# Performance work log

Hardware: AMD Instinct MI355X
Metric: run time of the kernel (lower is better)

## Reference

```python
import jax, jax.numpy as jnp
import numpy as np

EPS = 1.0  # global `epsilon` in the original code
B, C, N, T = 4, 32, 256, 288
NUM_PRED, NUM_LOCAL = 12, 12
PERIOD, SHORT, LONG = 24, 12, 48
EMB = 16
RE_K = 5  # ResidualExtrapolate kernel width (num_input)


def const_extrap(x, p):
    # replicate-pad right by p along time
    return jnp.concatenate([x, jnp.repeat(x[..., -1:], p, axis=-1)], axis=-1)


def seasonal_extrap(x, p):
    # circular-pad right by p along time (p <= t)
    return jnp.concatenate([x, x[..., :p]], axis=-1)


def term_norm(x, L):
    # sliding-window mean/var over last axis, window L, replicate-padded left.
    pad1 = [(0, 0)] * 3 + [(1, 0)]
    cs = jnp.pad(jnp.cumsum(x, axis=-1), pad1)
    cs2 = jnp.pad(jnp.cumsum(x * x, axis=-1), pad1)
    mean = (cs[..., L:] - cs[..., :-L]) / L            # (b,c,n,t-L+1)
    var = (cs2[..., L:] - cs2[..., :-L]) / L - mean ** 2 + 1e-5
    padL = [(0, 0)] * 3 + [(L - 1, 0)]
    mean = jnp.pad(mean, padL, mode='edge')
    var = jnp.pad(var, padL, mode='edge')
    out = (x - mean) / jnp.sqrt(var + EPS)
    return out, mean, jnp.sqrt(var)


def seasonal_norm(x, P):
    b, c, n, t = x.shape
    xp = x.reshape(b, c, n, t // P, P)
    mean = xp.mean(3)                                   # (b,c,n,P) per-phase
    var = (xp ** 2).mean(3) - mean ** 2 + 1e-5
    mean = jnp.tile(mean, (1, 1, 1, t // P))
    var = jnp.tile(var, (1, 1, 1, t // P))
    out = (x - mean) / jnp.sqrt(var + EPS)
    return out, mean, jnp.sqrt(var)


def spatial_norm(x, emb):
    n = emb.shape[0]
    adj = emb @ emb.T - 10.0 * jnp.eye(n, dtype=x.dtype)
    adj = jax.nn.softmax(adj, axis=-1)                  # (n,n)
    mean = jnp.einsum('nm,bcmt->bcnt', adj, x)
    var = jnp.einsum('nm,bcmt->bcnt', adj, x * x) - mean ** 2 + 1e-5
    out = (x - mean) / jnp.sqrt(var + EPS)
    return out, mean, jnp.sqrt(var)


def residual_extrap(x, W, bias):
    # Conv2d(c -> c*num_pred, kernel (1, RE_K)) on last RE_K steps, then cat.
    b, c, n, t = x.shape
    y = jnp.einsum('ock,bcnk->bon', W[:, :, 0, :], x[..., -RE_K:]) + bias[None, :, None]
    proj = y.reshape(b, NUM_PRED, c, n).transpose(0, 2, 3, 1)  # (b,c,n,num_pred)
    return jnp.concatenate([x, proj], axis=-1)


def conv_time(x, W, bias):
    y = jax.lax.conv_general_dilated(x, W, (1, 1), 'VALID',
                                     dimension_numbers=('NCHW', 'OIHW', 'NCHW'))
    return y + bias[None, :, None, None]


def conv1x1(x, W, bias):
    return jnp.einsum('oc,bcnt->bont', W[:, :, 0, 0], x) + bias[None, :, None, None]


def setup_inputs() -> dict:
    key = jax.random.key(0)
    ks = jax.random.split(key, 16)
    f32 = jnp.float32

    def w(k, shape, fan_in):
        return jax.random.normal(k, shape, dtype=f32) / np.sqrt(fan_in)

    inp = {
        'x': jax.random.normal(ks[0], (B, C, N, T), dtype=f32),
        'node_embedding': 0.1 * jax.random.normal(ks[1], (N, EMB), dtype=f32),
        'conv1_w': w(ks[6], (C, 13 * C, 1, NUM_LOCAL), 13 * C * NUM_LOCAL),
        'conv1_b': jnp.zeros((C,), f32),
        'conv2_w': w(ks[7], (C, 13 * C, 1, NUM_LOCAL), 13 * C * NUM_LOCAL),
        'conv2_b': jnp.zeros((C,), f32),
        'skip_w': w(ks[8], (C, C, 1, 1), C),
        'skip_b': jnp.zeros((C,), f32),
        'res_w': w(ks[9], (C, C, 1, 1), C),
        'res_b': jnp.zeros((C,), f32),
    }
    for i in range(4):
        inp[f're{i + 1}_w'] = w(ks[2 + i], (C * NUM_PRED, C, 1, RE_K), C * RE_K)
        inp[f're{i + 1}_b'] = jnp.zeros((C * NUM_PRED,), f32)
    return inp


def reference(x, node_embedding, conv1_w, conv1_b, conv2_w, conv2_b,
              skip_w, skip_b, res_w, res_b,
              re1_w, re1_b, re2_w, re2_b, re3_w, re3_b, re4_w, re4_b):
    xs, aux = [], []

    x_proj = const_extrap(x, NUM_PRED)
    zeros = jnp.zeros_like(x_proj)
    xs.append(x_proj); aux.append(zeros)

    x1, lt_mean, lt_std = term_norm(x, LONG)
    xp = residual_extrap(x1, re1_w, re1_b)
    mp, sp = const_extrap(lt_mean, NUM_PRED), const_extrap(lt_std, NUM_PRED)
    xs += [xp, mp, sp]; aux += [zeros, mp, sp]

    x2, se_mean, se_std = seasonal_norm(x1, PERIOD)
    xp = residual_extrap(x2, re2_w, re2_b)
    mp, sp = seasonal_extrap(se_mean, NUM_PRED), seasonal_extrap(se_std, NUM_PRED)
    xs += [xp, mp, sp]; aux += [zeros, mp, sp]

    x3, st_mean, st_std = term_norm(x2, SHORT)
    xp = residual_extrap(x3, re3_w, re3_b)
    mp, sp = const_extrap(st_mean, NUM_PRED), const_extrap(st_std, NUM_PRED)
    xs += [xp, mp, sp]; aux += [zeros, mp, sp]

    x4, sn_mean, sn_std = spatial_norm(x3, node_embedding)
    xp = residual_extrap(x4, re4_w, re4_b)
    mp, sp = const_extrap(sn_mean, NUM_PRED), const_extrap(sn_std, NUM_PRED)
    xs += [xp, mp, sp]; aux += [zeros, mp, sp]

    pad1 = [(0, 0)] * 3 + [(1, 0)]
    x_cat = jnp.pad(jnp.concatenate(xs, axis=1), pad1)      # (b,13c,n,T+P+1)
    a_cat = jnp.pad(jnp.concatenate(aux, axis=1), pad1)

    g1 = conv_time(x_cat, conv1_w, conv1_b)
    g2 = conv_time(x_cat, conv2_w, conv2_b)
    a1 = conv_time(a_cat, conv1_w, conv1_b)
    a2 = conv_time(a_cat, conv2_w, conv2_b)

    prod = g1 * g2
    x_z = conv1x1(prod[..., :-NUM_PRED], res_w, res_b)
    s = conv1x1(prod[..., -NUM_PRED:], skip_w, skip_b)
    s_aux = conv1x1((a1 * a2)[..., -NUM_PRED:], skip_w, skip_b)
    return (x_z, s_aux, s)
```

## Files before the change

### kernel.cpp

```cpp
#include <hip/hip_runtime.h>

typedef unsigned short u16;
typedef __attribute__((ext_vector_type(8))) short short8v;
typedef __attribute__((ext_vector_type(4))) float f32x4;

#define PSTR 304L
#define OFF_SAUX 9109504L
#define OFF_S    9502720L
#define CHSTR (32L*256L*PSTR)

static __device__ __forceinline__ float bf2f(u16 u) {
  return __uint_as_float(((unsigned int)u) << 16);
}
static __device__ __forceinline__ u16 f2bf(float f) {
  unsigned int i = __float_as_uint(f);
  i += 0x7FFFu + ((i >> 16) & 1u);
  return (u16)(i >> 16);
}

static __device__ __forceinline__ void gload16(const void* g, void* l) {
  __builtin_amdgcn_global_load_lds(
      (const __attribute__((address_space(1))) unsigned int*)g,
      (__attribute__((address_space(3))) unsigned int*)l, 16, 0, 0);
}

static __device__ void adj_body(int row, const float* __restrict__ emb,
                                u16* __restrict__ adjb) {
  const int m = threadIdx.x;
  __shared__ float sred[8];
  float er[16];
#pragma unroll
  for (int e = 0; e < 16; ++e) er[e] = emb[row * 16 + e];
  float d = 0.f;
#pragma unroll
  for (int e = 0; e < 16; ++e) d += er[e] * emb[m * 16 + e];
  if (m == row) d -= 10.f;
  float v = d;
#pragma unroll
  for (int off = 32; off; off >>= 1) v = fmaxf(v, __shfl_xor(v, off, 64));
  const int wid = m >> 6, lane = m & 63;
  if (lane == 0) sred[wid] = v;
  __syncthreads();
  const float mx = fmaxf(fmaxf(sred[0], sred[1]), fmaxf(sred[2], sred[3]));
  const float p = expf(d - mx);
  v = p;
#pragma unroll
  for (int off = 32; off; off >>= 1) v += __shfl_xor(v, off, 64);
  if (lane == 0) sred[4 + wid] = v;
  __syncthreads();
  const float sum = sred[4] + sred[5] + sred[6] + sred[7];
  adjb[row * 256 + m] = f2bf(p / sum);
}

static __device__ void prepw_body(int bid, const float* __restrict__ c1w,
                                  const float* __restrict__ c2w,
                                  u16* __restrict__ wB) {
  const int idx = bid * 256 + threadIdx.x;
  const int kk = idx >> 11;
  const int rem = idx & 2047;
  const int j = rem >> 5, chp = rem & 31;
  const int pslot = chp >> 3, chlo = chp & 7;
  const int sl = pslot ^ ((j >> 1) & 3);
  const int ch = sl * 8 + chlo;
  const int g = kk / 12, k = kk - g * 12;
  const int cin = g * 32 + ch;
  const float* src = (j < 32) ? c1w : c2w;
  const int jj = j & 31;
  wB[idx] = f2bf(src[(jj * 416 + cin) * 12 + k]);
}

static __device__ __forceinline__ void wscan2(float& s1, float& s2, int lane) {
#pragma unroll
  for (int off = 1; off < 64; off <<= 1) {
    float a = __shfl_up(s1, off, 64);
    float b = __shfl_up(s2, off, 64);
    if (lane >= off) { s1 += a; s2 += b; }
  }
}

static __device__ void norm_body(int bid, const float* __restrict__ x,
                                 u16* __restrict__ xcat) {
  const int wid = threadIdx.x >> 6, lane = threadIdx.x & 63;
  const long row = (long)bid * 4 + wid;
  const int b = (int)(row >> 13);
  const int c = (int)((row >> 8) & 31);
  const int n = (int)(row & 255);
  const float* xr = x + row * 288;
  __shared__ float bufA[4][304], bufB[4][304], cs1[4][312], cs2[4][312], sst[4][80];
  float* bA = bufA[wid];
  float* bB = bufB[wid];
  float* p1 = cs1[wid];
  float* p2 = cs2[wid];
  float* psm = sst[wid];
  float* psi = sst[wid] + 24;
  float* psd = sst[wid] + 48;
  const long chb = (long)b * 416 * 256 + n;

  for (int j = 0; j < 5; ++j) { int t = j * 64 + lane; if (t < 288) bA[t] = xr[t]; }

  auto scanbuf = [&](float* src) {
    float ca = 0.f, cb = 0.f;
    if (lane == 0) { p1[0] = 0.f; p2[0] = 0.f; }
    for (int j = 0; j < 5; ++j) {
      int t = j * 64 + lane;
      float v = (t < 288) ? src[t] : 0.f;
      float s1 = v, s2 = v * v;
      wscan2(s1, s2, lane);
      if (t < 288) { p1[t + 1] = ca + s1; p2[t + 1] = cb + s2; }
      ca += __shfl(s1, 63, 64);
      cb += __shfl(s2, 63, 64);
    }
  };

  scanbuf(bA);
  for (int j = 0; j < 5; ++j) {
    int t = j * 64 + lane; if (t >= 288) continue;
    float S, Q;
    if (t >= 47) { S = p1[t + 1] - p1[t - 47]; Q = p2[t + 1] - p2[t - 47]; }
    else         { S = p1[48];                 Q = p2[48]; }
    float m = S * (1.f / 48.f);
    float var = Q * (1.f / 48.f) - m * m + 1e-5f;
    float sd = sqrtf(var);
    float iv = rsqrtf(var + 1.f);
    float xv = bA[t];
    float x1 = (xv - m) * iv;
    bB[t] = x1;
    xcat[(chb + (long)(c)      * 256) * PSTR + 1 + t] = f2bf(xv);
    xcat[(chb + (long)(32 + c) * 256) * PSTR + 1 + t] = f2bf(x1);
    xcat[(chb + (long)(64 + c) * 256) * PSTR + 1 + t] = f2bf(m);
    xcat[(chb + (long)(96 + c) * 256) * PSTR + 1 + t] = f2bf(sd);
  }
  {
    float S = p1[288] - p1[240], Q = p2[288] - p2[240];
    float m = S * (1.f / 48.f);
    float var = Q * (1.f / 48.f) - m * m + 1e-5f;
    float sd = sqrtf(var);
    if (lane < 12) {
      xcat[(chb + (long)(c)      * 256) * PSTR + 289 + lane] = f2bf(bA[287]);
      xcat[(chb + (long)(64 + c) * 256) * PSTR + 289 + lane] = f2bf(m);
      xcat[(chb + (long)(96 + c) * 256) * PSTR + 289 + lane] = f2bf(sd);
    }
    if (lane == 0) {
      xcat[(chb + (long)(c)      * 256) * PSTR] = 0;
      xcat[(chb + (long)(32 + c) * 256) * PSTR] = 0;
      xcat[(chb + (long)(64 + c) * 256) * PSTR] = 0;
      xcat[(chb + (long)(96 + c) * 256) * PSTR] = 0;
    }
  }
  if (lane < 24) {
    float S = 0.f, Q = 0.f;
#pragma unroll
    for (int i2 = 0; i2 < 12; ++i2) { float v = bB[lane + 24 * i2]; S += v; Q += v * v; }
    float m = S * (1.f / 12.f);
    float var = Q * (1.f / 12.f) - m * m + 1e-5f;
    psm[lane] = m; psi[lane] = rsqrtf(var + 1.f); psd[lane] = sqrtf(var);
  }
  for (int j = 0; j < 5; ++j) {
    int t = j * 64 + lane; if (t >= 288) continue;
    int ph = t % 24;
    float m = psm[ph];
    float x2v = (bB[t] - m) * psi[ph];
    bA[t] = x2v;
    xcat[(chb + (long)(128 + c) * 256) * PSTR + 1 + t] = f2bf(x2v);
    xcat[(chb + (long)(160 + c) * 256) * PSTR + 1 + t] = f2bf(m);
    xcat[(chb + (long)(192 + c) * 256) * PSTR + 1 + t] = f2bf(psd[ph]);
  }
  if (lane < 12) {
    xcat[(chb + (long)(160 + c) * 256) * PSTR + 289 + lane] = f2bf(psm[lane]);
    xcat[(chb + (long)(192 + c) * 256) * PSTR + 289 + lane] = f2bf(psd[lane]);
  }
  if (lane == 0) {
    xcat[(chb + (long)(128 + c) * 256) * PSTR] = 0;
    xcat[(chb + (long)(160 + c) * 256) * PSTR] = 0;
    xcat[(chb + (long)(192 + c) * 256) * PSTR] = 0;
  }
  scanbuf(bA);
  for (int j = 0; j < 5; ++j) {
    int t = j * 64 + lane; if (t >= 288) continue;
    float S, Q;
    if (t >= 11) { S = p1[t + 1] - p1[t - 11]; Q = p2[t + 1] - p2[t - 11]; }
    else         { S = p1[12];                 Q = p2[12]; }
    float m = S * (1.f / 12.f);
    float var = Q * (1.f / 12.f) - m * m + 1e-5f;
    float sd = sqrtf(var);
    float iv = rsqrtf(var + 1.f);
    float x3v = (bA[t] - m) * iv;
    xcat[(chb + (long)(224 + c) * 256) * PSTR + 1 + t] = f2bf(x3v);
    xcat[(chb + (long)(256 + c) * 256) * PSTR + 1 + t] = f2bf(m);
    xcat[(chb + (long)(288 + c) * 256) * PSTR + 1 + t] = f2bf(sd);
  }
  {
    float S = p1[288] - p1[276], Q = p2[288] - p2[276];
    float m = S * (1.f / 12.f);
    float var = Q * (1.f / 12.f) - m * m + 1e-5f;
    float sd = sqrtf(var);
    if (lane < 12) {
      xcat[(chb + (long)(256 + c) * 256) * PSTR + 289 + lane] = f2bf(m);
      xcat[(chb + (long)(288 + c) * 256) * PSTR + 289 + lane] = f2bf(sd);
    }
    if (lane == 0) {
      xcat[(chb + (long)(224 + c) * 256) * PSTR] = 0;
      xcat[(chb + (long)(256 + c) * 256) * PSTR] = 0;
      xcat[(chb + (long)(288 + c) * 256) * PSTR] = 0;
    }
  }
}

__global__ __launch_bounds__(256) void k_front(const float* __restrict__ x,
    const float* __restrict__ emb, const float* __restrict__ c1w,
    const float* __restrict__ c2w, u16* __restrict__ xcat,
    u16* __restrict__ adjb, u16* __restrict__ wB) {
  const int bid = blockIdx.x;
  if (bid < 8192)       norm_body(bid, x, xcat);
  else if (bid < 8448)  adj_body(bid - 8192, emb, adjb);
  else                  prepw_body(bid - 8448, c1w, c2w, wB);
}

static __device__ void re_body(long gid, u16* __restrict__ xcat,
                               const float* __restrict__ W,
                               const float* __restrict__ bias, int srcch) {
  const int o = (int)(gid % 384);
  const long bn = gid / 384;
  const int n = (int)(bn & 255);
  const int b = (int)(bn >> 8);
  const float* wr = W + o * 160;
  float acc = bias[o];
  for (int c = 0; c < 32; ++c) {
    const long rb = ((long)(b * 416 + srcch + c) * 256 + n) * PSTR + 284;
#pragma unroll
    for (int k = 0; k < 5; ++k) acc += wr[c * 5 + k] * bf2f(xcat[rb + k]);
  }
  const int cd = o & 31, p = o >> 5;
  xcat[((long)(b * 416 + srcch + cd) * 256 + n) * PSTR + 289 + p] = f2bf(acc);
}

__global__ __launch_bounds__(256) void k_re4(u16* __restrict__ xcat,
                                             const float* __restrict__ W,
                                             const float* __restrict__ bias) {
  re_body((long)blockIdx.x * 256 + threadIdx.x, xcat, W, bias, 320);
}

static __device__ void spatial_body(int sid, u16* __restrict__ xcat,
                                    const u16* __restrict__ adjb) {
  const int gx = sid % 20;
  const int slice = sid / 20;
  const int tcn = gx >> 2, ncb = gx & 3;
  const int b = slice >> 5, c = slice & 31;
  const int t0 = tcn * 64, n0 = ncb * 64;
  const int tid = threadIdx.x;
  const int wid = tid >> 6, lane = tid & 63;
  const int wm = wid >> 1, wn = wid & 1;
  const int l15 = lane & 15, lq = lane >> 4;
  __shared__ __align__(16) u16 BT[2][64 * 40];
  __shared__ __align__(16) u16 BT2[2][64 * 40];
  const f32x4 vz = {0.f, 0.f, 0.f, 0.f};
  f32x4 aM[2][2], aV[2][2];
#pragma unroll
  for (int i = 0; i < 2; ++i)
#pragma unroll
    for (int j = 0; j < 2; ++j) { aM[i][j] = vz; aV[i][j] = vz; }
  const long base7 = (long)(b * 416 + 224 + c) * 256;
  u16 rv[8];
#pragma unroll
  for (int r = 0; r < 8; ++r) {
    int idx = tid + r * 256; int ml = idx >> 6, s = idx & 63;
    rv[r] = xcat[(base7 + ml) * PSTR + 1 + t0 + s];
  }
#pragma unroll
  for (int r = 0; r < 8; ++r) {
    int idx = tid + r * 256; int ml = idx >> 6, s = idx & 63;
    float v = bf2f(rv[r]);
    BT[0][s * 40 + ml] = rv[r];
    BT2[0][s * 40 + ml] = f2bf(v * v);
  }
  __syncthreads();
  int cur = 0;
  for (int kk = 0; kk < 8; ++kk) {
    u16 rn[8];
    if (kk < 7) {
#pragma unroll
      for (int r = 0; r < 8; ++r) {
        int idx = tid + r * 256; int ml = idx >> 6, s = idx & 63;
        rn[r] = xcat[(base7 + (long)((kk + 1) * 32 + ml)) * PSTR + 1 + t0 + s];
      }
    }
    const short8v a0 = *(const short8v*)(adjb + (long)(n0 + wm * 32 + l15) * 256 + kk * 32 + lq * 8);
    const short8v a1 = *(const short8v*)(adjb + (long)(n0 + wm * 32 + 16 + l15) * 256 + kk * 32 + lq * 8);
    const u16* bt = BT[cur];
    const u16* bq = BT2[cur];
    const short8v b0 = *(const short8v*)(bt + (wn * 32 + l15) * 40 + lq * 8);
    const short8v b1 = *(const short8v*)(bt + (wn * 32 + 16 + l15) * 40 + lq * 8);
    const short8v q0 = *(const short8v*)(bq + (wn * 32 + l15) * 40 + lq * 8);
    const short8v q1 = *(const short8v*)(bq + (wn * 32 + 16 + l15) * 40 + lq * 8);
    aM[0][0] = __builtin_amdgcn_mfma_f32_16x16x32_bf16(a0, b0, aM[0][0], 0, 0, 0);
    aM[0][1] = __builtin_amdgcn_mfma_f32_16x16x32_bf16(a0, b1, aM[0][1], 0, 0, 0);
    aM[1][0] = __builtin_amdgcn_mfma_f32_16x16x32_bf16(a1, b0, aM[1][0], 0, 0, 0);
    aM[1][1] = __builtin_amdgcn_mfma_f32_16x16x32_bf16(a1, b1, aM[1][1], 0, 0, 0);
    aV[0][0] = __builtin_amdgcn_mfma_f32_16x16x32_bf16(a0, q0, aV[0][0], 0, 0, 0);
    aV[0][1] = __builtin_amdgcn_mfma_f32_16x16x32_bf16(a0, q1, aV[0][1], 0, 0, 0);
    aV[1][0] = __builtin_amdgcn_mfma_f32_16x16x32_bf16(a1, q0, aV[1][0], 0, 0, 0);
    aV[1][1] = __builtin_amdgcn_mfma_f32_16x16x32_bf16(a1, q1, aV[1][1], 0, 0, 0);
    __syncthreads();
    if (kk < 7) {
#pragma unroll
      for (int r = 0; r < 8; ++r) {
        int idx = tid + r * 256; int ml = idx >> 6, s = idx & 63;
        float v = bf2f(rn[r]);
        BT[cur ^ 1][s * 40 + ml] = rn[r];
        BT2[cur ^ 1][s * 40 + ml] = f2bf(v * v);
      }
    }
    __syncthreads();
    cur ^= 1;
  }
#pragma unroll
  for (int mf = 0; mf < 2; ++mf)
#pragma unroll
    for (int nf = 0; nf < 2; ++nf)
#pragma unroll
      for (int e = 0; e < 4; ++e) {
        const int i = wm * 32 + mf * 16 + lq * 4 + e;
        const int j = wn * 32 + nf * 16 + l15;
        const int nn = n0 + i, tt2 = t0 + j;
        if (tt2 < 288) {
          const float mean = aM[mf][nf][e], ex2 = aV[mf][nf][e];
          const float var = ex2 - mean * mean + 1e-5f;
          const float sd = sqrtf(var);
          const float iv = rsqrtf(var + 1.f);
          const float x3c = bf2f(xcat[(base7 + nn) * PSTR + 1 + tt2]);
          const float x4 = (x3c - mean) * iv;
          const long r10 = ((long)(b * 416 + 320 + c) * 256 + nn) * PSTR;
          const long r11 = ((long)(b * 416 + 352 + c) * 256 + nn) * PSTR;
          const long r12 = ((long)(b * 416 + 384 + c) * 256 + nn) * PSTR;
          xcat[r10 + 1 + tt2] = f2bf(x4);
          xcat[r11 + 1 + tt2] = f2bf(mean);
          xcat[r12 + 1 + tt2] = f2bf(sd);
          if (tt2 == 287) {
            for (int p = 0; p < 12; ++p) {
              xcat[r11 + 289 + p] = f2bf(mean);
              xcat[r12 + 289 + p] = f2bf(sd);
            }
          }
          if (tt2 == 0) { xcat[r10] = 0; xcat[r11] = 0; xcat[r12] = 0; }
        }
      }
}

__global__ __launch_bounds__(256) void k_mid(u16* __restrict__ xcat,
    const u16* __restrict__ adjb,
    const float* __restrict__ w1, const float* __restrict__ b1,
    const float* __restrict__ w2, const float* __restrict__ b2,
    const float* __restrict__ w3, const float* __restrict__ b3) {
  const int bid = blockIdx.x;
  if (bid < 2560) { spatial_body(bid, xcat, adjb); return; }
  const int sub = bid - 2560;
  const int which = sub / 1536;
  const long gid = (long)(sub - which * 1536) * 256 + threadIdx.x;
  if (which == 0)      re_body(gid, xcat, w1, b1, 32);
  else if (which == 1) re_body(gid, xcat, w2, b2, 128);
  else                 re_body(gid, xcat, w3, b3, 224);
}

__global__ __launch_bounds__(256, 3) void k_convG(
    const u16* __restrict__ xcat, const u16* __restrict__ wB,
    const float* __restrict__ c1b, const float* __restrict__ c2b,
    const float* __restrict__ rsw, const float* __restrict__ rsb,
    const float* __restrict__ skw, const float* __restrict__ skb,
    float* __restrict__ out) {
  const int bid = blockIdx.x;
  const int xcd = bid & 7;
  const int i5 = bid >> 3;
  const int by = xcd * 32 + i5 / 5;
  const int tc = i5 % 5;
  const int b = by >> 6;
  const int tid = threadIdx.x;
  const int wid = tid >> 6, lane = tid & 63;
  const int n_abs = (by & 63) * 4 + wid;
  const int t0 = tc * 64;
  const int l15 = lane & 15, lq = lane >> 4;

  __shared__ __align__(16) unsigned char smem[41984];
  u16* Asm = (u16*)smem;
  u16* Bsm = (u16*)(smem + 25600);

  int sch[5], stk[5];
  const u16* baseR[5];
#pragma unroll
  for (int r = 0; r < 5; ++r) {
    int cc = r * 64 + lane;
    int s = cc / 10;
    int tk = cc - s * 10;
    sch[r] = s; stk[r] = tk;
    baseR[r] = xcat + ((long)(b * 416 + s) * 256 + n_abs) * PSTR + t0 + tk * 8;
  }
  u16* aw = Asm + wid * 3200;

#define AWRITE() { \
    _Pragma("unroll") \
    for (int r = 0; r < 5; ++r) { \
      u16 pc[8]; *(uint4*)pc = aR[r]; \
      const int pcol = ((((sch[r] >> 3) ^ stk[r]) & 3) << 3) + (sch[r] & 7); \
      _Pragma("unroll") \
      for (int e = 0; e < 8; ++e) aw[(stk[r] * 8 + e) * 40 + pcol] = pc[e]; \
    } }

  uint4 aR[5];
#pragma unroll
  for (int r = 0; r < 5; ++r) aR[r] = *(const uint4*)baseR[r];
  AWRITE();
#pragma unroll
  for (int r = 0; r < 5; ++r) aR[r] = *(const uint4*)(baseR[r] + CHSTR);
  gload16(wB + 0 * 2048 + wid * 512 + lane * 8, Bsm + 0 + wid * 512);
  gload16(wB + 1 * 2048 + wid * 512 + lane * 8, Bsm + 2048 + wid * 512);
  __syncthreads();

  const f32x4 vz = {0.f, 0.f, 0.f, 0.f};
  f32x4 acc[4][4];
#pragma unroll
  for (int i = 0; i < 4; ++i)
#pragma unroll
    for (int j = 0; j < 4; ++j) acc[i][j] = vz;

  const u16* bwl = Bsm + l15 * 32 + ((lq ^ ((l15 >> 1) & 3)) << 3);

  int p = 0;
  for (int g = 0; g < 13; ++g) {
    for (int kp = 0; kp < 6; ++kp) {
      if (p < 77) {
        const long kkn = (long)(p + 1) * 2;
        const int bufn = ((p + 1) & 1) * 4096;
        gload16(wB + kkn * 2048 + wid * 512 + lane * 8, Bsm + bufn + wid * 512);
        gload16(wB + (kkn + 1) * 2048 + wid * 512 + lane * 8, Bsm + bufn + 2048 + wid * 512);
      }
      const int bufc = (p & 1) * 4096;
#pragma unroll
      for (int kh = 0; kh < 2; ++kh) {
        const int K = kp * 2 + kh;
        short8v af[4], bf[4];
#pragma unroll
        for (int f = 0; f < 4; ++f) {
          const int tt = K + f * 16 + l15;
          af[f] = *(const short8v*)(aw + tt * 40 + (((lq ^ (tt >> 3)) & 3) << 3));
        }
#pragma unroll
        for (int f = 0; f < 4; ++f)
          bf[f] = *(const short8v*)(bwl + bufc + kh * 2048 + f * 512);
#pragma unroll
        for (int i = 0; i < 4; ++i)
#pragma unroll
          for (int j = 0; j < 4; ++j)
            acc[i][j] = __builtin_amdgcn_mfma_f32_16x16x32_bf16(af[i], bf[j], acc[i][j], 0, 0, 0);
      }
      __syncthreads();
      ++p;
    }
    if (g < 12) {
      AWRITE();
      if (g < 11) {
#pragma unroll
        for (int r = 0; r < 5; ++r) aR[r] = *(const uint4*)(baseR[r] + (long)(g + 2) * CHSTR);
      }
    }
  }
#undef AWRITE
  __syncthreads();

  float* pw = (float*)smem + wid * 2112;
#pragma unroll
  for (int fi = 0; fi < 4; ++fi)
#pragma unroll
    for (int nf = 0; nf < 2; ++nf)
#pragma unroll
      for (int e = 0; e < 4; ++e) {
        const int trow = fi * 16 + lq * 4 + e;
        const int cch = nf * 16 + l15;
        const float g1 = acc[fi][nf][e] + c1b[cch];
        const float g2 = acc[fi][nf + 2][e] + c2b[cch];
        pw[trow * 33 + cch] = g1 * g2;
      }
  float pv[32];
  {
    const float* prow = pw + lane * 33;
#pragma unroll
    for (int c = 0; c < 32; ++c) pv[c] = prow[c];
  }
  const int t = t0 + lane;
  if (t0 + 63 < 278) {
    for (int o = 0; o < 32; ++o) {
      float s = rsb[o];
      const float* wr = rsw + o * 32;
#pragma unroll
      for (int c = 0; c < 32; ++c) s += wr[c] * pv[c];
      out[((long)(b * 32 + o) * 256 + n_abs) * 278 + t] = s;
    }
  } else {
    const bool isres = t < 278;
    const bool isskip = (t >= 278) && (t < 290);
    for (int o = 0; o < 32; ++o) {
      const float* wr = (isres ? rsw : skw) + o * 32;
      float s = (isres ? rsb : skb)[o];
#pragma unroll
      for (int c = 0; c < 32; ++c) s += wr[c] * pv[c];
      if (isres)       out[((long)(b * 32 + o) * 256 + n_abs) * 278 + t] = s;
      else if (isskip) out[OFF_S + ((long)(b * 32 + o) * 256 + n_abs) * 12 + (t - 278)] = s;
    }
  }
}

__global__ __launch_bounds__(256) void k_convA(const u16* __restrict__ xcat,
    const u16* __restrict__ wB, const float* __restrict__ c1b,
    const float* __restrict__ c2b, const float* __restrict__ skw,
    const float* __restrict__ skb, float* __restrict__ out) {
  const int tid = threadIdx.x;
  const int wid = tid >> 6, lane = tid & 63;
  const int row = blockIdx.x * 4 + wid;
  const int b = row >> 8, n = row & 255;
  const int l15 = lane & 15, lq = lane >> 4;
  __shared__ __align__(16) u16 ATa[4][32 * 40];
  __shared__ float apL[4][16 * 65];
  u16* at = ATa[wid];
  float* ap = apL[wid];
  const f32x4 vz = {0.f, 0.f, 0.f, 0.f};
  f32x4 acc[4] = {vz, vz, vz, vz};
  const long bnbase = (long)b * 416 * 256 + n;
  const int bsw = (lq ^ ((l15 >> 1) & 3)) << 3;
  for (int gi = 0; gi < 8; ++gi) {
    const int g = 2 + 3 * (gi >> 1) + (gi & 1);
#pragma unroll
    for (int r = 0; r < 14; ++r) {
      int idx = lane + r * 64;
      int ci = idx / 28, s = idx - ci * 28;
      at[s * 40 + ci] = xcat[(bnbase + (long)(g * 32 + ci) * 256) * PSTR + 278 + s];
    }
    for (int k = 0; k < 12; ++k) {
      const short8v af = *(const short8v*)(at + (l15 + k) * 40 + lq * 8);
#pragma unroll
      for (int nf = 0; nf < 4; ++nf) {
        const short8v bf = *(const short8v*)(wB + (long)(g * 12 + k) * 2048 + (nf * 16 + l15) * 32 + bsw);
        acc[nf] = __builtin_amdgcn_mfma_f32_16x16x32_bf16(af, bf, acc[nf], 0, 0, 0);
      }
    }
  }
#pragma unroll
  for (int nf = 0; nf < 4; ++nf)
#pragma unroll
    for (int e = 0; e < 4; ++e)
      ap[(lq * 4 + e) * 65 + nf * 16 + l15] = acc[nf][e];
  for (int r = 0; r < 6; ++r) {
    const int task = lane + r * 64;
    const int o = task & 31, tt = task >> 5;
    float s = skb[o];
#pragma unroll
    for (int c2 = 0; c2 < 32; ++c2)
      s += skw[o * 32 + c2] * (ap[tt * 65 + c2] + c1b[c2]) * (ap[tt * 65 + 32 + c2] + c2b[c2]);
    out[OFF_SAUX + ((long)(b * 32 + o) * 256 + n) * 12 + tt] = s;
  }
}

extern "C" void kernel_launch(void* const* d_in, const int* in_sizes, int n_in,
                              void* d_out, int out_size, void* d_ws, size_t ws_size,
                              hipStream_t stream) {
  const float* x   = (const float*)d_in[0];
  const float* emb = (const float*)d_in[1];
  const float* c1w = (const float*)d_in[2];
  const float* c1b = (const float*)d_in[3];
  const float* c2w = (const float*)d_in[4];
  const float* c2b = (const float*)d_in[5];
  const float* skw = (const float*)d_in[6];
  const float* skb = (const float*)d_in[7];
  const float* rsw = (const float*)d_in[8];
  const float* rsb = (const float*)d_in[9];
  float* out = (float*)d_out;

  u16* xcat = (u16*)d_ws;
  u16* wB   = xcat + (4L * 416 * 256 * 304 + 2048);
  u16* adjb = wB + 156L * 2048;

  k_front<<<dim3(9696), dim3(256), 0, stream>>>(x, emb, c1w, c2w, xcat, adjb, wB);
  k_mid<<<dim3(7168), dim3(256), 0, stream>>>(xcat, adjb,
      (const float*)d_in[10], (const float*)d_in[11],
      (const float*)d_in[12], (const float*)d_in[13],
      (const float*)d_in[14], (const float*)d_in[15]);
  k_re4<<<dim3(1536), dim3(256), 0, stream>>>(xcat, (const float*)d_in[16], (const float*)d_in[17]);
  k_convG<<<dim3(1280), dim3(256), 0, stream>>>(xcat, wB, c1b, c2b, rsw, rsb, skw, skb, out);
  k_convA<<<dim3(256), dim3(256), 0, stream>>>(xcat, wB, c1b, c2b, skw, skb, out);
}
```

Measured before the change: 748.8 us.

## Split aux conv over channel groups per block, use vector loads, simplify convG grid

k_convA now gives each (b,n) row its own block and splits the 8 channel groups across the four waves, two groups per wave. Partial MFMA accumulators are then reduced through shared memory before the skip projection. Input tiles are fetched with 16-byte vector loads starting at an aligned offset, replacing scalar gathers. This raises parallelism for the small aux kernel from 256 to 1024 blocks. k_convG also drops its XCD-aware block swizzle for a plain 2D grid, which may hurt L2 locality across chiplets.

```diff
diff --git a/kernel.cpp b/kernel.cpp
--- a/kernel.cpp
+++ b/kernel.cpp
@@ -367,11 +367,8 @@
     const float* __restrict__ rsw, const float* __restrict__ rsb,
     const float* __restrict__ skw, const float* __restrict__ skb,
     float* __restrict__ out) {
-  const int bid = blockIdx.x;
-  const int xcd = bid & 7;
-  const int i5 = bid >> 3;
-  const int by = xcd * 32 + i5 / 5;
-  const int tc = i5 % 5;
+  const int tc = blockIdx.x;
+  const int by = blockIdx.y;
   const int b = by >> 6;
   const int tid = threadIdx.x;
   const int wid = tid >> 6, lane = tid & 63;
@@ -513,27 +510,39 @@
     const float* __restrict__ skb, float* __restrict__ out) {
   const int tid = threadIdx.x;
   const int wid = tid >> 6, lane = tid & 63;
-  const int row = blockIdx.x * 4 + wid;
+  const int row = blockIdx.x;
   const int b = row >> 8, n = row & 255;
   const int l15 = lane & 15, lq = lane >> 4;
-  __shared__ __align__(16) u16 ATa[4][32 * 40];
-  __shared__ float apL[4][16 * 65];
-  u16* at = ATa[wid];
-  float* ap = apL[wid];
+  __shared__ __align__(16) u16 ATa[4][2][36 * 40];
+  __shared__ float apL[4][16 * 68];
+  const int gtab[8] = {2, 3, 5, 6, 8, 9, 11, 12};
+  const long bnbase = (long)b * 416 * 256 + n;
+
+#pragma unroll
+  for (int tau = 0; tau < 2; ++tau) {
+    const int g = gtab[wid * 2 + tau];
+    u16* at = ATa[wid][tau];
+#pragma unroll
+    for (int h = 0; h < 2; ++h) {
+      const int c = lane + h * 64;
+      const int ch = c >> 2, part = c & 3;
+      const uint4 v = *(const uint4*)(xcat +
+          (bnbase + (long)(g * 32 + ch) * 256) * PSTR + 272 + part * 8);
+      u16 pc[8]; *(uint4*)pc = v;
+#pragma unroll
+      for (int e = 0; e < 8; ++e) at[(part * 8 + e) * 40 + ch] = pc[e];
+    }
+  }
+
   const f32x4 vz = {0.f, 0.f, 0.f, 0.f};
   f32x4 acc[4] = {vz, vz, vz, vz};
-  const long bnbase = (long)b * 416 * 256 + n;
   const int bsw = (lq ^ ((l15 >> 1) & 3)) << 3;
-  for (int gi = 0; gi < 8; ++gi) {
-    const int g = 2 + 3 * (gi >> 1) + (gi & 1);
-#pragma unroll
-    for (int r = 0; r < 14; ++r) {
-      int idx = lane + r * 64;
-      int ci = idx / 28, s = idx - ci * 28;
-      at[s * 40 + ci] = xcat[(bnbase + (long)(g * 32 + ci) * 256) * PSTR + 278 + s];
-    }
+#pragma unroll
+  for (int tau = 0; tau < 2; ++tau) {
+    const int g = gtab[wid * 2 + tau];
+    const u16* at = ATa[wid][tau];
     for (int k = 0; k < 12; ++k) {
-      const short8v af = *(const short8v*)(at + (l15 + k) * 40 + lq * 8);
+      const short8v af = *(const short8v*)(at + (l15 + k + 6) * 40 + lq * 8);
 #pragma unroll
       for (int nf = 0; nf < 4; ++nf) {
         const short8v bf = *(const short8v*)(wB + (long)(g * 12 + k) * 2048 + (nf * 16 + l15) * 32 + bsw);
@@ -541,18 +550,26 @@
       }
     }
   }
+  float* ap = apL[wid];
 #pragma unroll
   for (int nf = 0; nf < 4; ++nf)
 #pragma unroll
     for (int e = 0; e < 4; ++e)
-      ap[(lq * 4 + e) * 65 + nf * 16 + l15] = acc[nf][e];
-  for (int r = 0; r < 6; ++r) {
-    const int task = lane + r * 64;
+      ap[(lq * 4 + e) * 68 + nf * 16 + l15] = acc[nf][e];
+  __syncthreads();
+  for (int idx = tid; idx < 1024; idx += 256) {
+    const int m = idx >> 6, j = idx & 63;
+    apL[0][m * 68 + j] = apL[0][m * 68 + j] + apL[1][m * 68 + j]
+                       + apL[2][m * 68 + j] + apL[3][m * 68 + j];
+  }
+  __syncthreads();
+  for (int task = tid; task < 384; task += 256) {
     const int o = task & 31, tt = task >> 5;
     float s = skb[o];
 #pragma unroll
     for (int c2 = 0; c2 < 32; ++c2)
-      s += skw[o * 32 + c2] * (ap[tt * 65 + c2] + c1b[c2]) * (ap[tt * 65 + 32 + c2] + c2b[c2]);
+      s += skw[o * 32 + c2] * (apL[0][tt * 68 + c2] + c1b[c2])
+                            * (apL[0][tt * 68 + 32 + c2] + c2b[c2]);
     out[OFF_SAUX + ((long)(b * 32 + o) * 256 + n) * 12 + tt] = s;
   }
 }
@@ -582,6 +599,6 @@
       (const float*)d_in[12], (const float*)d_in[13],
       (const float*)d_in[14], (const float*)d_in[15]);
   k_re4<<<dim3(1536), dim3(256), 0, stream>>>(xcat, (const float*)d_in[16], (const float*)d_in[17]);
-  k_convG<<<dim3(1280), dim3(256), 0, stream>>>(xcat, wB, c1b, c2b, rsw, rsb, skw, skb, out);
-  k_convA<<<dim3(256), dim3(256), 0, stream>>>(xcat, wB, c1b, c2b, skw, skb, out);
-}
+  k_convG<<<dim3(5, 256), dim3(256), 0, stream>>>(xcat, wB, c1b, c2b, rsw, rsb, skw, skb, out);
+  k_convA<<<dim3(1024), dim3(256), 0, stream>>>(xcat, wB, c1b, c2b, skw, skb, out);
+}
```

New measurement: 676.7 us. 1.11x faster.
